# Kernel tuning notes

Measured on AMD Instinct MI355X. Metric: run time of the kernel, lower is better.

Reference implementation:

```python
import jax, jax.numpy as jnp
import numpy as np

N_HEAD = 16
THETA = 10000.0


def _rope_cos_sin(T, head_dim):
    # freqs: (T, head_dim//2), matches torch.polar(ones, outer(t, 1/theta^(2i/d)))
    inv = 1.0 / (THETA ** (jnp.arange(0, head_dim, 2, dtype=jnp.float32) / head_dim))
    freqs = jnp.arange(T, dtype=jnp.float32)[:, None] * inv[None, :]
    # broadcast shape (1, T, 1, head_dim//2) over (B, T, H, head_dim//2)
    return jnp.cos(freqs)[None, :, None, :], jnp.sin(freqs)[None, :, None, :]


def _apply_rope(t, cos, sin):
    # t: (B, T, H, hd); pairs (even, odd) form complex numbers
    B, T, H, hd = t.shape
    tr = t.astype(jnp.float32).reshape(B, T, H, hd // 2, 2)
    re, im = tr[..., 0], tr[..., 1]
    out = jnp.stack([re * cos - im * sin, re * sin + im * cos], axis=-1)
    return out.reshape(B, T, H, hd).astype(t.dtype)


def setup_inputs() -> dict:
    key = jax.random.key(0)
    k1, k2, k3 = jax.random.split(key, 3)
    C = 1024
    x = jax.random.normal(k1, (4, 2048, C), dtype=jnp.float32)
    w_attn = jax.random.normal(k2, (3 * C, C), dtype=jnp.float32) * 0.02
    w_proj = jax.random.normal(k3, (C, C), dtype=jnp.float32) * 0.02
    return {"x": x, "w_attn": w_attn, "w_proj": w_proj}


def reference(x, w_attn, w_proj):
    B, T, C = x.shape
    H = N_HEAD
    hd = C // H
    qkv = x @ w_attn.T  # (B, T, 3C) fused QKV projection
    q, k, v = jnp.split(qkv, 3, axis=-1)
    q = q.reshape(B, T, H, hd)
    k = k.reshape(B, T, H, hd)
    v = v.reshape(B, T, H, hd).transpose(0, 2, 1, 3)  # (B, H, T, hd)
    cos, sin = _rope_cos_sin(T, hd)
    q = _apply_rope(q, cos, sin).transpose(0, 2, 1, 3)  # (B, H, T, hd)
    k = _apply_rope(k, cos, sin).transpose(0, 2, 1, 3)
    scale = 1.0 / jnp.sqrt(jnp.float32(hd))
    scores = jnp.einsum('bhqd,bhkd->bhqk', q, k) * scale
    attn = jax.nn.softmax(scores, axis=-1)
    y = jnp.einsum('bhqk,bhkd->bhqd', attn, v)  # (B, H, T, hd)
    y = y.transpose(0, 2, 1, 3).reshape(B, T, C)
    return y @ w_proj.T
```

## Files before the change

### kernel.cpp

```cpp
#include <hip/hip_runtime.h>
#include <math.h>

#define BATCH 4
#define TSEQ 2048
#define CDIM 1024
#define NHEAD 16
#define HDIM 64
#define M_ROWS (BATCH * TSEQ)

typedef float f32x4 __attribute__((ext_vector_type(4)));
typedef __bf16 bf16x8 __attribute__((ext_vector_type(8)));
typedef unsigned int u32x4 __attribute__((ext_vector_type(4)));

typedef const __attribute__((address_space(1))) void gas_void;
typedef __attribute__((address_space(3))) void las_void;

static __device__ __forceinline__ unsigned short f2bf(float f) {
    unsigned int x = __float_as_uint(f);
    x += 0x7fffu + ((x >> 16) & 1u);
    return (unsigned short)(x >> 16);
}

__global__ void cvt_bf16_kernel(const float* __restrict__ in, unsigned short* __restrict__ out, int n) {
    int i = (blockIdx.x * blockDim.x + threadIdx.x) << 3;
    if (i >= n) return;
    float4 a = *(const float4*)(in + i);
    float4 b = *(const float4*)(in + i + 4);
    union { unsigned short u[8]; u32x4 v; } pk;
    pk.u[0] = f2bf(a.x); pk.u[1] = f2bf(a.y); pk.u[2] = f2bf(a.z); pk.u[3] = f2bf(a.w);
    pk.u[4] = f2bf(b.x); pk.u[5] = f2bf(b.y); pk.u[6] = f2bf(b.z); pk.u[7] = f2bf(b.w);
    *(u32x4*)(out + i) = pk.v;
}

__global__ void rope_table_kernel(float* __restrict__ cosT, float* __restrict__ sinT) {
    int idx = blockIdx.x * blockDim.x + threadIdx.x;
    if (idx >= TSEQ * (HDIM / 2)) return;
    int t = idx >> 5;
    int i = idx & 31;
    double inv = pow(10000.0, -((double)(2 * i)) / (double)HDIM);
    double ph = (double)t * inv;
    cosT[idx] = (float)cos(ph);
    sinT[idx] = (float)sin(ph);
}

#define GROW(p) (((p) & 64) + (((p) & 15) << 2) + (((p) >> 4) & 3))
#define GEMM_CORE(A_, B_, K_, bm_, bn_)                                          \
    const int tid = threadIdx.x;                                                 \
    const int w = tid >> 6, lane = tid & 63;                                     \
    const int l15 = lane & 15, quad = lane >> 4;                                 \
    const int wm = w >> 1, wn = w & 1;                                           \
    const int srow = (w << 5) + (lane >> 2);                                     \
    const int kpart = (lane & 3) << 3;                                           \
    const unsigned short* Ag0 = A_ + (size_t)(bm_ + srow) * K_ + kpart;          \
    const unsigned short* Ag1 = A_ + (size_t)(bm_ + srow + 16) * K_ + kpart;     \
    const unsigned short* Bg0 = B_ + (size_t)(bn_ + GROW(srow)) * K_ + kpart;    \
    const unsigned short* Bg1 = B_ + (size_t)(bn_ + GROW(srow + 16)) * K_ + kpart; \
    unsigned short* Al0 = As + srow * 32 + kpart;                                \
    unsigned short* Al1 = As + (srow + 16) * 32 + kpart;                         \
    unsigned short* Bl0 = Bs + srow * 32 + kpart;                                \
    unsigned short* Bl1 = Bs + (srow + 16) * 32 + kpart;                         \
    f32x4 acc[4][4];                                                             \
    _Pragma("unroll")                                                            \
    for (int i = 0; i < 4; ++i)                                                  \
        _Pragma("unroll")                                                        \
        for (int j = 0; j < 4; ++j) acc[i][j] = (f32x4){0.f, 0.f, 0.f, 0.f};     \
    for (int k0 = 0; k0 < K_; k0 += 32) {                                        \
        __builtin_amdgcn_global_load_lds((gas_void*)(Ag0 + k0), (las_void*)Al0, 16, 0, 0); \
        __builtin_amdgcn_global_load_lds((gas_void*)(Ag1 + k0), (las_void*)Al1, 16, 0, 0); \
        __builtin_amdgcn_global_load_lds((gas_void*)(Bg0 + k0), (las_void*)Bl0, 16, 0, 0); \
        __builtin_amdgcn_global_load_lds((gas_void*)(Bg1 + k0), (las_void*)Bl1, 16, 0, 0); \
        __syncthreads();                                                         \
        bf16x8 af[4], bf[4];                                                     \
        _Pragma("unroll")                                                        \
        for (int mi = 0; mi < 4; ++mi)                                           \
            af[mi] = __builtin_bit_cast(bf16x8,                                  \
                *(const u32x4*)(As + ((wm << 6) + (mi << 4) + l15) * 32 + (quad << 3))); \
        _Pragma("unroll")                                                        \
        for (int ni = 0; ni < 4; ++ni)                                           \
            bf[ni] = __builtin_bit_cast(bf16x8,                                  \
                *(const u32x4*)(Bs + ((wn << 6) + (ni << 4) + l15) * 32 + (quad << 3))); \
        _Pragma("unroll")                                                        \
        for (int mi = 0; mi < 4; ++mi)                                           \
            _Pragma("unroll")                                                    \
            for (int ni = 0; ni < 4; ++ni)                                       \
                acc[mi][ni] = __builtin_amdgcn_mfma_f32_16x16x32_bf16(af[mi], bf[ni], acc[mi][ni], 0, 0, 0); \
        __syncthreads();                                                         \
    }

__global__ __launch_bounds__(256) void gemm_qkv_fused(
        const unsigned short* __restrict__ A, const unsigned short* __restrict__ B,
        unsigned short* __restrict__ qb, unsigned short* __restrict__ kb,
        unsigned short* __restrict__ vb,
        const float* __restrict__ cosT, const float* __restrict__ sinT) {
    __shared__ __align__(16) unsigned short As[128 * 32];
    __shared__ __align__(16) unsigned short Bs[128 * 32];
    const int bm = blockIdx.y << 7;
    const int bn = blockIdx.x << 7;
    GEMM_CORE(A, B, CDIM, bm, bn)

    const int nbase = bn + (wn << 6);
    const int mbase = bm + (wm << 6);
    const int b = mbase >> 11;
    const int tt0 = mbase & (TSEQ - 1);
    const int d0 = l15 << 2;
    const int fi = l15 << 1;

    if (nbase < 2 * CDIM) {
        const int isQ = (nbase < CDIM) ? 1 : 0;
        unsigned short* dst = isQ ? qb : kb;
        const float qs = isQ ? 0.18033688f : 1.0f;
        const int h = (nbase & (CDIM - 1)) >> 6;
        unsigned short* hb = dst + (size_t)(b * NHEAD + h) * TSEQ * HDIM;
#pragma unroll
        for (int mi = 0; mi < 4; ++mi) {
#pragma unroll
            for (int r = 0; r < 4; ++r) {
                const int t = tt0 + (mi << 4) + (quad << 2) + r;
                float2 cc = *(const float2*)(cosT + (t << 5) + fi);
                float2 ss = *(const float2*)(sinT + (t << 5) + fi);
                float re0 = acc[mi][0][r], im0 = acc[mi][1][r];
                float re1 = acc[mi][2][r], im1 = acc[mi][3][r];
                union { unsigned short u[4]; uint2 v; } pk;
                pk.u[0] = f2bf((re0 * cc.x - im0 * ss.x) * qs);
                pk.u[1] = f2bf((re0 * ss.x + im0 * cc.x) * qs);
                pk.u[2] = f2bf((re1 * cc.y - im1 * ss.y) * qs);
                pk.u[3] = f2bf((re1 * ss.y + im1 * cc.y) * qs);
                *(uint2*)(hb + (size_t)t * HDIM + d0) = pk.v;
            }
        }
    } else {
        const int h = (nbase - 2 * CDIM) >> 6;
        unsigned short* hb = vb + (size_t)(b * NHEAD + h) * HDIM * TSEQ;
#pragma unroll
        for (int mi = 0; mi < 4; ++mi) {
            const int t0 = tt0 + (mi << 4) + (quad << 2);
#pragma unroll
            for (int ni = 0; ni < 4; ++ni) {
                const int d = d0 + ni;
                union { unsigned short u[4]; uint2 v; } pk;
#pragma unroll
                for (int r = 0; r < 4; ++r) pk.u[r] = f2bf(acc[mi][ni][r]);
                *(uint2*)(hb + (size_t)d * TSEQ + t0) = pk.v;
            }
        }
    }
}

__global__ __launch_bounds__(256) void gemm_proj(
        const unsigned short* __restrict__ A, const unsigned short* __restrict__ B,
        float* __restrict__ C) {
    __shared__ __align__(16) unsigned short As[128 * 32];
    __shared__ __align__(16) unsigned short Bs[128 * 32];
    const int bm = blockIdx.y << 7;
    const int bn = blockIdx.x << 7;
    GEMM_CORE(A, B, CDIM, bm, bn)

#pragma unroll
    for (int mi = 0; mi < 4; ++mi)
#pragma unroll
        for (int r = 0; r < 4; ++r) {
            const int row = bm + (wm << 6) + (mi << 4) + (quad << 2) + r;
            float4 v = make_float4(acc[mi][0][r], acc[mi][1][r], acc[mi][2][r], acc[mi][3][r]);
            *(float4*)(C + (size_t)row * CDIM + bn + (wn << 6) + (l15 << 2)) = v;
        }
}

#define KTILE 64
#define NKT (TSEQ / KTILE)
#define QBLK 256
#define SWZ(row, ch) (((row) << 6) + ((((ch) ^ ((row) & 7))) << 3))
__global__ __launch_bounds__(256, 2) void attn_mfma(
        const unsigned short* __restrict__ qb, const unsigned short* __restrict__ kb,
        const unsigned short* __restrict__ vb, unsigned short* __restrict__ y) {
    const int bh = blockIdx.x;
    const int qt = blockIdx.y;
    const int b = bh >> 4, h = bh & 15;
    const int tid  = threadIdx.x;
    const int w    = tid >> 6;
    const int lane = tid & 63;
    const int l15  = lane & 15;
    const int quad = lane >> 4;

    __shared__ __align__(16) unsigned short Ks[KTILE * 64];
    __shared__ __align__(16) unsigned short Vs[HDIM * 64];
    __shared__ __align__(16) unsigned short Ps[4][64 * 64];

    const size_t qoff = ((size_t)bh * TSEQ + qt * QBLK + w * 64) * HDIM;
    bf16x8 aq[4][2];
#pragma unroll
    for (int mt = 0; mt < 4; ++mt)
#pragma unroll
        for (int kc2 = 0; kc2 < 2; ++kc2) {
            u32x4 v = *(const u32x4*)(qb + qoff + (size_t)(mt * 16 + l15) * HDIM + kc2 * 32 + quad * 8);
            aq[mt][kc2] = __builtin_bit_cast(bf16x8, v);
        }

    f32x4 o[4][4];
    float l_r[4][4];
#pragma unroll
    for (int mt = 0; mt < 4; ++mt)
#pragma unroll
        for (int nc = 0; nc < 4; ++nc) o[mt][nc] = (f32x4){0.f, 0.f, 0.f, 0.f};
#pragma unroll
    for (int mt = 0; mt < 4; ++mt)
#pragma unroll
        for (int r = 0; r < 4; ++r) l_r[mt][r] = 0.f;

    const unsigned short* kbase = kb + (size_t)bh * TSEQ * HDIM;
    const unsigned short* vbase = vb + (size_t)bh * HDIM * TSEQ;

    const int sr = tid >> 3;
    const int sp = (tid & 7) << 3;
    const int pp0 = ((sr & 3) << 4) + (sr >> 2);
    const int st0 = SWZ(pp0, tid & 7);
    const int st1 = SWZ(pp0 + 8, tid & 7);

    u32x4 kr[2], vr[2];
#pragma unroll
    for (int l = 0; l < 2; ++l) {
        int idx = sr + (l << 5);
        kr[l] = *(const u32x4*)(kbase + (size_t)idx * HDIM + sp);
        vr[l] = *(const u32x4*)(vbase + (size_t)idx * TSEQ + sp);
    }

    for (int kt = 0; kt < NKT; ++kt) {
        __syncthreads();
        *(u32x4*)&Ks[st0] = kr[0];
        *(u32x4*)&Ks[st1] = kr[1];
        *(u32x4*)&Vs[st0] = vr[0];
        *(u32x4*)&Vs[st1] = vr[1];
        if (kt + 1 < NKT) {
            int base = (kt + 1) * KTILE;
#pragma unroll
            for (int l = 0; l < 2; ++l) {
                int idx = sr + (l << 5);
                kr[l] = *(const u32x4*)(kbase + (size_t)(base + idx) * HDIM + sp);
                vr[l] = *(const u32x4*)(vbase + (size_t)idx * TSEQ + base + sp);
            }
        }
        __syncthreads();

        f32x4 s[4][4];
#pragma unroll
        for (int nc = 0; nc < 4; ++nc) {
            const int rowK = nc * 16 + l15;
            u32x4 k0 = *(const u32x4*)&Ks[SWZ(rowK, quad)];
            u32x4 k1 = *(const u32x4*)&Ks[SWZ(rowK, quad ^ 4)];
            bf16x8 bk0 = __builtin_bit_cast(bf16x8, k0);
            bf16x8 bk1 = __builtin_bit_cast(bf16x8, k1);
#pragma unroll
            for (int mt = 0; mt < 4; ++mt) {
                f32x4 a2 = (f32x4){0.f, 0.f, 0.f, 0.f};
                a2 = __builtin_amdgcn_mfma_f32_16x16x32_bf16(aq[mt][0], bk0, a2, 0, 0, 0);
                a2 = __builtin_amdgcn_mfma_f32_16x16x32_bf16(aq[mt][1], bk1, a2, 0, 0, 0);
                s[mt][nc] = a2;
            }
        }

#pragma unroll
        for (int mt = 0; mt < 4; ++mt)
#pragma unroll
            for (int r = 0; r < 4; ++r) {
                float p0 = __builtin_amdgcn_exp2f(s[mt][0][r]);
                float p1 = __builtin_amdgcn_exp2f(s[mt][1][r]);
                float p2 = __builtin_amdgcn_exp2f(s[mt][2][r]);
                float p3 = __builtin_amdgcn_exp2f(s[mt][3][r]);
                l_r[mt][r] += (p0 + p1) + (p2 + p3);
                uint2 pk;
                pk.x = __builtin_amdgcn_perm(__float_as_uint(p1), __float_as_uint(p0), 0x07060302u);
                pk.y = __builtin_amdgcn_perm(__float_as_uint(p3), __float_as_uint(p2), 0x07060302u);
                const int rowP = mt * 16 + quad * 4 + r;
                *(uint2*)&Ps[w][SWZ(rowP, l15 >> 1) + ((l15 & 1) << 2)] = pk;
            }
        __threadfence_block();

        bf16x8 ap[4][2];
#pragma unroll
        for (int mt = 0; mt < 4; ++mt)
#pragma unroll
            for (int kc2 = 0; kc2 < 2; ++kc2) {
                const int rowP = mt * 16 + l15;
                u32x4 v = *(const u32x4*)&Ps[w][SWZ(rowP, kc2 * 4 + quad)];
                ap[mt][kc2] = __builtin_bit_cast(bf16x8, v);
            }
#pragma unroll
        for (int nc = 0; nc < 4; ++nc) {
            const int rowV = nc * 16 + l15;
            u32x4 v0 = *(const u32x4*)&Vs[SWZ(rowV, quad)];
            u32x4 v1 = *(const u32x4*)&Vs[SWZ(rowV, quad ^ 4)];
            bf16x8 bv0 = __builtin_bit_cast(bf16x8, v0);
            bf16x8 bv1 = __builtin_bit_cast(bf16x8, v1);
#pragma unroll
            for (int mt = 0; mt < 4; ++mt) {
                o[mt][nc] = __builtin_amdgcn_mfma_f32_16x16x32_bf16(ap[mt][0], bv0, o[mt][nc], 0, 0, 0);
                o[mt][nc] = __builtin_amdgcn_mfma_f32_16x16x32_bf16(ap[mt][1], bv1, o[mt][nc], 0, 0, 0);
            }
        }
    }

#pragma unroll
    for (int off = 1; off < 16; off <<= 1)
#pragma unroll
        for (int mt = 0; mt < 4; ++mt)
#pragma unroll
            for (int r = 0; r < 4; ++r)
                l_r[mt][r] += __shfl_xor(l_r[mt][r], off, 64);

#pragma unroll
    for (int mt = 0; mt < 4; ++mt)
#pragma unroll
        for (int r = 0; r < 4; ++r) {
            float inv_l = 1.f / l_r[mt][r];
            int t = qt * QBLK + w * 64 + mt * 16 + quad * 4 + r;
            unsigned short* row = y + (size_t)(b * TSEQ + t) * CDIM + h * HDIM;
            union { unsigned short u[4]; uint2 v; } pk;
#pragma unroll
            for (int nc = 0; nc < 4; ++nc) pk.u[nc] = f2bf(o[mt][nc][r] * inv_l);
            *(uint2*)(row + (l15 << 2)) = pk.v;
        }
}

extern "C" void kernel_launch(void* const* d_in, const int* in_sizes, int n_in,
                              void* d_out, int out_size, void* d_ws, size_t ws_size,
                              hipStream_t stream) {
    const float* x      = (const float*)d_in[0];
    const float* w_attn = (const float*)d_in[1];
    const float* w_proj = (const float*)d_in[2];
    float* out = (float*)d_out;

    unsigned short* xb  = (unsigned short*)d_ws;
    unsigned short* wab = xb  + (size_t)M_ROWS * CDIM;
    unsigned short* wpb = wab + (size_t)3 * CDIM * CDIM;
    unsigned short* qb  = wpb + (size_t)CDIM * CDIM;
    unsigned short* kb  = qb  + (size_t)BATCH * NHEAD * TSEQ * HDIM;
    unsigned short* vb  = kb  + (size_t)BATCH * NHEAD * TSEQ * HDIM;
    unsigned short* yb  = vb  + (size_t)BATCH * NHEAD * TSEQ * HDIM;
    float* cosT = (float*)(yb + (size_t)M_ROWS * CDIM);
    float* sinT = cosT + TSEQ * (HDIM / 2);

    cvt_bf16_kernel<<<(M_ROWS * CDIM / 8 + 255) / 256, 256, 0, stream>>>(x, xb, M_ROWS * CDIM);
    cvt_bf16_kernel<<<(3 * CDIM * CDIM / 8 + 255) / 256, 256, 0, stream>>>(w_attn, wab, 3 * CDIM * CDIM);
    cvt_bf16_kernel<<<(CDIM * CDIM / 8 + 255) / 256, 256, 0, stream>>>(w_proj, wpb, CDIM * CDIM);

    rope_table_kernel<<<(TSEQ * 32) / 256, 256, 0, stream>>>(cosT, sinT);

    dim3 g1(3 * CDIM / 128, M_ROWS / 128);
    gemm_qkv_fused<<<g1, 256, 0, stream>>>(xb, wab, qb, kb, vb, cosT, sinT);

    dim3 g2(BATCH * NHEAD, TSEQ / QBLK);
    attn_mfma<<<g2, 256, 0, stream>>>(qb, kb, vb, yb);

    dim3 g3(CDIM / 128, M_ROWS / 128);
    gemm_proj<<<g3, 256, 0, stream>>>(yb, wpb, out);
}
```

Measured before the change: 279.7 us.

## Double-buffer K/V tiles in attention, add MFMA priority, merge prep kernels

The attention kernel now keeps two shared-memory buffers for K and V. The next tile is written into the idle buffer after the QK^T MFMAs, which leaves one barrier per iteration instead of two. s_setprio raises wave priority around the MFMA blocks so issue can interleave across waves. Separately, the three bf16 conversion launches and the rope-table launch are merged into a single prep kernel to cut launch overhead. Double buffering adds 16 KB of LDS per block, which may lower occupancy under launch_bounds(256,2).

Result: no change. 276.6 us (-1.1%).

```diff
diff --git a/kernel.cpp b/kernel.cpp
--- a/kernel.cpp
+++ b/kernel.cpp
@@ -21,26 +21,34 @@
     return (unsigned short)(x >> 16);
 }
 
-__global__ void cvt_bf16_kernel(const float* __restrict__ in, unsigned short* __restrict__ out, int n) {
-    int i = (blockIdx.x * blockDim.x + threadIdx.x) << 3;
-    if (i >= n) return;
-    float4 a = *(const float4*)(in + i);
-    float4 b = *(const float4*)(in + i + 4);
-    union { unsigned short u[8]; u32x4 v; } pk;
-    pk.u[0] = f2bf(a.x); pk.u[1] = f2bf(a.y); pk.u[2] = f2bf(a.z); pk.u[3] = f2bf(a.w);
-    pk.u[4] = f2bf(b.x); pk.u[5] = f2bf(b.y); pk.u[6] = f2bf(b.z); pk.u[7] = f2bf(b.w);
-    *(u32x4*)(out + i) = pk.v;
-}
-
-__global__ void rope_table_kernel(float* __restrict__ cosT, float* __restrict__ sinT) {
-    int idx = blockIdx.x * blockDim.x + threadIdx.x;
-    if (idx >= TSEQ * (HDIM / 2)) return;
-    int t = idx >> 5;
-    int i = idx & 31;
-    double inv = pow(10000.0, -((double)(2 * i)) / (double)HDIM);
-    double ph = (double)t * inv;
-    cosT[idx] = (float)cos(ph);
-    sinT[idx] = (float)sin(ph);
+__global__ void prep_kernel(const float* __restrict__ x, unsigned short* __restrict__ xb,
+                            const float* __restrict__ wa, unsigned short* __restrict__ wab,
+                            const float* __restrict__ wp, unsigned short* __restrict__ wpb,
+                            float* __restrict__ cosT, float* __restrict__ sinT) {
+    int blk = blockIdx.x;
+    if (blk < 6144) {
+        const float* in;
+        unsigned short* out;
+        int base;
+        if (blk < 4096)      { in = x;  out = xb;  base = blk; }
+        else if (blk < 5632) { in = wa; out = wab; base = blk - 4096; }
+        else                 { in = wp; out = wpb; base = blk - 5632; }
+        int i = (base * 256 + threadIdx.x) << 3;
+        float4 a = *(const float4*)(in + i);
+        float4 b = *(const float4*)(in + i + 4);
+        union { unsigned short u[8]; u32x4 v; } pk;
+        pk.u[0] = f2bf(a.x); pk.u[1] = f2bf(a.y); pk.u[2] = f2bf(a.z); pk.u[3] = f2bf(a.w);
+        pk.u[4] = f2bf(b.x); pk.u[5] = f2bf(b.y); pk.u[6] = f2bf(b.z); pk.u[7] = f2bf(b.w);
+        *(u32x4*)(out + i) = pk.v;
+    } else {
+        int idx = (blk - 6144) * 256 + threadIdx.x;
+        int t = idx >> 5;
+        int i = idx & 31;
+        double inv = pow(10000.0, -((double)(2 * i)) / (double)HDIM);
+        double ph = (double)t * inv;
+        cosT[idx] = (float)cos(ph);
+        sinT[idx] = (float)sin(ph);
+    }
 }
 
 #define GROW(p) (((p) & 64) + (((p) & 15) << 2) + (((p) >> 4) & 3))
@@ -181,8 +189,8 @@
     const int l15  = lane & 15;
     const int quad = lane >> 4;
 
-    __shared__ __align__(16) unsigned short Ks[KTILE * 64];
-    __shared__ __align__(16) unsigned short Vs[HDIM * 64];
+    __shared__ __align__(16) unsigned short Ks[2][KTILE * 64];
+    __shared__ __align__(16) unsigned short Vs[2][HDIM * 64];
     __shared__ __align__(16) unsigned short Ps[4][64 * 64];
 
     const size_t qoff = ((size_t)bh * TSEQ + qt * QBLK + w * 64) * HDIM;
@@ -222,30 +230,28 @@
         kr[l] = *(const u32x4*)(kbase + (size_t)idx * HDIM + sp);
         vr[l] = *(const u32x4*)(vbase + (size_t)idx * TSEQ + sp);
     }
+    *(u32x4*)&Ks[0][st0] = kr[0];
+    *(u32x4*)&Ks[0][st1] = kr[1];
+    *(u32x4*)&Vs[0][st0] = vr[0];
+    *(u32x4*)&Vs[0][st1] = vr[1];
+#pragma unroll
+    for (int l = 0; l < 2; ++l) {
+        int idx = sr + (l << 5);
+        kr[l] = *(const u32x4*)(kbase + (size_t)(KTILE + idx) * HDIM + sp);
+        vr[l] = *(const u32x4*)(vbase + (size_t)idx * TSEQ + KTILE + sp);
+    }
 
     for (int kt = 0; kt < NKT; ++kt) {
+        const int cur = kt & 1;
         __syncthreads();
-        *(u32x4*)&Ks[st0] = kr[0];
-        *(u32x4*)&Ks[st1] = kr[1];
-        *(u32x4*)&Vs[st0] = vr[0];
-        *(u32x4*)&Vs[st1] = vr[1];
-        if (kt + 1 < NKT) {
-            int base = (kt + 1) * KTILE;
-#pragma unroll
-            for (int l = 0; l < 2; ++l) {
-                int idx = sr + (l << 5);
-                kr[l] = *(const u32x4*)(kbase + (size_t)(base + idx) * HDIM + sp);
-                vr[l] = *(const u32x4*)(vbase + (size_t)idx * TSEQ + base + sp);
-            }
-        }
-        __syncthreads();
 
         f32x4 s[4][4];
+        __builtin_amdgcn_s_setprio(1);
 #pragma unroll
         for (int nc = 0; nc < 4; ++nc) {
             const int rowK = nc * 16 + l15;
-            u32x4 k0 = *(const u32x4*)&Ks[SWZ(rowK, quad)];
-            u32x4 k1 = *(const u32x4*)&Ks[SWZ(rowK, quad ^ 4)];
+            u32x4 k0 = *(const u32x4*)&Ks[cur][SWZ(rowK, quad)];
+            u32x4 k1 = *(const u32x4*)&Ks[cur][SWZ(rowK, quad ^ 4)];
             bf16x8 bk0 = __builtin_bit_cast(bf16x8, k0);
             bf16x8 bk1 = __builtin_bit_cast(bf16x8, k1);
 #pragma unroll
@@ -254,6 +260,24 @@
                 a2 = __builtin_amdgcn_mfma_f32_16x16x32_bf16(aq[mt][0], bk0, a2, 0, 0, 0);
                 a2 = __builtin_amdgcn_mfma_f32_16x16x32_bf16(aq[mt][1], bk1, a2, 0, 0, 0);
                 s[mt][nc] = a2;
+            }
+        }
+        __builtin_amdgcn_s_setprio(0);
+
+        if (kt + 1 < NKT) {
+            const int nxt = cur ^ 1;
+            *(u32x4*)&Ks[nxt][st0] = kr[0];
+            *(u32x4*)&Ks[nxt][st1] = kr[1];
+            *(u32x4*)&Vs[nxt][st0] = vr[0];
+            *(u32x4*)&Vs[nxt][st1] = vr[1];
+            if (kt + 2 < NKT) {
+                int base = (kt + 2) * KTILE;
+#pragma unroll
+                for (int l = 0; l < 2; ++l) {
+                    int idx = sr + (l << 5);
+                    kr[l] = *(const u32x4*)(kbase + (size_t)(base + idx) * HDIM + sp);
+                    vr[l] = *(const u32x4*)(vbase + (size_t)idx * TSEQ + base + sp);
+                }
             }
         }
 
@@ -283,11 +307,12 @@
                 u32x4 v = *(const u32x4*)&Ps[w][SWZ(rowP, kc2 * 4 + quad)];
                 ap[mt][kc2] = __builtin_bit_cast(bf16x8, v);
             }
+        __builtin_amdgcn_s_setprio(1);
 #pragma unroll
         for (int nc = 0; nc < 4; ++nc) {
             const int rowV = nc * 16 + l15;
-            u32x4 v0 = *(const u32x4*)&Vs[SWZ(rowV, quad)];
-            u32x4 v1 = *(const u32x4*)&Vs[SWZ(rowV, quad ^ 4)];
+            u32x4 v0 = *(const u32x4*)&Vs[cur][SWZ(rowV, quad)];
+            u32x4 v1 = *(const u32x4*)&Vs[cur][SWZ(rowV, quad ^ 4)];
             bf16x8 bv0 = __builtin_bit_cast(bf16x8, v0);
             bf16x8 bv1 = __builtin_bit_cast(bf16x8, v1);
 #pragma unroll
@@ -296,6 +321,7 @@
                 o[mt][nc] = __builtin_amdgcn_mfma_f32_16x16x32_bf16(ap[mt][1], bv1, o[mt][nc], 0, 0, 0);
             }
         }
+        __builtin_amdgcn_s_setprio(0);
     }
 
 #pragma unroll
@@ -338,11 +364,7 @@
     float* cosT = (float*)(yb + (size_t)M_ROWS * CDIM);
     float* sinT = cosT + TSEQ * (HDIM / 2);
 
-    cvt_bf16_kernel<<<(M_ROWS * CDIM / 8 + 255) / 256, 256, 0, stream>>>(x, xb, M_ROWS * CDIM);
-    cvt_bf16_kernel<<<(3 * CDIM * CDIM / 8 + 255) / 256, 256, 0, stream>>>(w_attn, wab, 3 * CDIM * CDIM);
-    cvt_bf16_kernel<<<(CDIM * CDIM / 8 + 255) / 256, 256, 0, stream>>>(w_proj, wpb, CDIM * CDIM);
-
-    rope_table_kernel<<<(TSEQ * 32) / 256, 256, 0, stream>>>(cosT, sinT);
+    prep_kernel<<<6400, 256, 0, stream>>>(x, xb, w_attn, wab, w_proj, wpb, cosT, sinT);
 
     dim3 g1(3 * CDIM / 128, M_ROWS / 128);
     gemm_qkv_fused<<<g1, 256, 0, stream>>>(xb, wab, qb, kb, vb, cosT, sinT);
```
